# Kernel optimization log

Hardware: AMD Instinct MI355X
Metric: run time of the kernel (lower is better)

The kernel has to match this reference:

```python
import jax, jax.numpy as jnp
import numpy as np

G = 4      # groups (conv groups == offset groups)
KS = 3     # kernel size
DIL = 1    # dilation
PAD = 1    # padding = dilation
EPS = 1e-5 # InstanceNorm eps


def setup_inputs() -> dict:
    key = jax.random.key(0)
    k1, k2, k3, k4, k5 = jax.random.split(key, 5)
    B, C, D, H, W = 4, 64, 8, 64, 64
    Cout = 64
    Cg = C // G
    x = jax.random.normal(k1, (B, C, D, H, W), jnp.float32)
    # small offset-conv weights so predicted offsets stay within a few pixels
    w_off = jax.random.normal(k2, (2 * KS * KS * G, Cg, KS, KS), jnp.float32) * 0.01
    b_off = jax.random.normal(k3, (2 * KS * KS * G,), jnp.float32) * 0.01
    w_dc = jax.random.normal(k4, (Cout, Cg, KS, KS), jnp.float32) * (1.0 / np.sqrt(Cg * KS * KS))
    b_dc = jax.random.normal(k5, (Cout,), jnp.float32) * 0.01
    return {"x": x, "w_off": w_off, "b_off": b_off, "w_dc": w_dc, "b_dc": b_dc}


def reference(x, w_off, b_off, w_dc, b_dc):
    B, C, D, H, W = x.shape
    N = B * D
    K = KS * KS
    Cg = C // G
    # torch .view(B*D, C, H, W) is a row-major reshape of the flat buffer
    x2 = x.reshape(N, C, H, W)

    # grouped 3x3 offset conv, same padding
    off = jax.lax.conv_general_dilated(
        x2, w_off, (1, 1), [(PAD, PAD), (PAD, PAD)],
        rhs_dilation=(DIL, DIL), feature_group_count=G,
        dimension_numbers=("NCHW", "OIHW", "NCHW"),
    ) + b_off[None, :, None, None]
    off = off.reshape(N, G, K, 2, H, W)        # (y, x) offset per group/kernel-pt
    dy, dx = off[:, :, :, 0], off[:, :, :, 1]  # [N,G,K,H,W]

    # base sampling grid per kernel point
    ki, kj = jnp.meshgrid(jnp.arange(KS), jnp.arange(KS), indexing="ij")
    ki = ki.reshape(K); kj = kj.reshape(K)
    base_y = (jnp.arange(H)[None, :] - PAD + ki[:, None] * DIL).astype(jnp.float32)  # [K,H]
    base_x = (jnp.arange(W)[None, :] - PAD + kj[:, None] * DIL).astype(jnp.float32)  # [K,W]
    py = base_y[None, None, :, :, None] + dy   # [N,G,K,H,W]
    px = base_x[None, None, :, None, :] + dx

    y0 = jnp.floor(py); x0 = jnp.floor(px)
    ly = py - y0; lx = px - x0
    y0i = y0.astype(jnp.int32); x0i = x0.astype(jnp.int32)

    xg = x2.reshape(N, G, Cg, H * W)
    gather = jax.vmap(jax.vmap(lambda xf, idx: xf[:, idx]))  # over N, G

    def corner(yi, xi, w):
        valid = (yi >= 0) & (yi < H) & (xi >= 0) & (xi < W)   # zero-pad OOB
        idx = jnp.clip(yi, 0, H - 1) * W + jnp.clip(xi, 0, W - 1)
        v = gather(xg, idx.reshape(N, G, -1)).reshape(N, G, Cg, K, H, W)
        return v * (w * valid)[:, :, None]                    # broadcast over Cg

    val = (corner(y0i,     x0i,     (1 - ly) * (1 - lx))
         + corner(y0i,     x0i + 1, (1 - ly) * lx)
         + corner(y0i + 1, x0i,     ly * (1 - lx))
         + corner(y0i + 1, x0i + 1, ly * lx))                 # [N,G,Cg,K,H,W]

    wg = w_dc.reshape(G, -1, Cg, K)                           # [G,Coutg,Cg,K]
    out = jnp.einsum("gock,ngckhw->ngohw", wg, val).reshape(N, -1, H, W)
    out = out + b_dc[None, :, None, None]

    # InstanceNorm2d (affine=False, biased var) + exact GELU
    m = out.mean((-2, -1), keepdims=True)
    v = out.var((-2, -1), keepdims=True)
    out = jax.nn.gelu((out - m) * jax.lax.rsqrt(v + EPS), approximate=False)

    Cout = out.shape[1]
    return out.reshape(B, D, Cout, H, W).transpose(0, 2, 1, 3, 4)  # [B,Cout,D,H,W]
```

## Files before the change

kernel.cpp:

```cpp
#include <hip/hip_runtime.h>
#include <hip/hip_fp16.h>
#include <math.h>

#define HW 4096
#define NN 32
#define W68 68
#define RSTR 2192

typedef __attribute__((ext_vector_type(8))) _Float16 f16x8;
typedef __attribute__((ext_vector_type(2))) _Float16 h2;
typedef __attribute__((ext_vector_type(4))) float f32x4;

__device__ inline unsigned short hbits(float a) {
    _Float16 h = (_Float16)a;
    unsigned short u;
    __builtin_memcpy(&u, &h, 2);
    return u;
}
__device__ inline unsigned hpack(float a, float b) {
    auto p = __builtin_amdgcn_cvt_pkrtz(a, b);
    unsigned u;
    __builtin_memcpy(&u, &p, 4);
    return u;
}

__device__ inline int xsw(int x, int c8) {
    return ((x << 5) | (c8 << 4)) ^ (((x >> 2) & 1) << 4);
}

__global__ __launch_bounds__(256) void wperm_build(const float* __restrict__ w_off,
                                                   const float* __restrict__ w_dc,
                                                   unsigned short* __restrict__ wperm)
{
    int idx = blockIdx.x * 256 + threadIdx.x;
    int g = idx / 7680;
    int r3 = idx - g * 7680;
    int which = r3 / 2560;
    int r = r3 - which * 2560;
    int j = r & 7;
    int rest = r >> 3;
    int nn_ = rest & 15; rest >>= 4;
    int q_ = rest & 3, kp_ = rest >> 2;
    int k = q_ * 8 + j;
    int c = k & 15, tt = kp_ * 2 + (k >> 4);
    float v = 0.f;
    if (tt < 9) {
        if (which == 0)      v = w_dc[(g * 16 + nn_) * 144 + c * 9 + tt];
        else if (which == 1) v = w_off[(g * 18 + nn_) * 144 + c * 9 + tt];
        else if (nn_ < 2)    v = w_off[(g * 18 + 16 + nn_) * 144 + c * 9 + tt];
    }
    wperm[idx] = hbits(v);
}

__global__ __launch_bounds__(256, 4) void fused_conv(const float* __restrict__ x,
                                                     const unsigned short* __restrict__ wperm,
                                                     const float* __restrict__ b_off,
                                                     const float* __restrict__ b_dc,
                                                     unsigned short* __restrict__ outpre)
{
    __shared__ __attribute__((aligned(16))) unsigned short xwin[9864];
    __shared__ __attribute__((aligned(16))) unsigned short off_lds[256 * 20];

    int bhw = blockIdx.x;
    int bx = (bhw & 7) * 256 + (bhw >> 3);
    int n = bx >> 6, g = (bx >> 4) & 3, chunk = bx & 15;
    int t = threadIdx.x;
    int lane = t & 63, wv = t >> 6;
    int nn = lane & 15, q = lane >> 4;
    int t2 = q >> 1, chh = q & 1;
    int R0 = chunk * 4;

    const unsigned short* wpg = wperm + g * 7680;
    const float* xgbase = x + (size_t)(n * 64 + g * 16) * HW;

    {
        int col = lane;
        #pragma unroll
        for (int rr = 0; rr < 2; rr++) {
            int r = wv * 2 + rr;
            int h = R0 + r - 2;
            uint4 lo = {0, 0, 0, 0}, hi = {0, 0, 0, 0};
            if ((unsigned)h < 64u) {
                const float* xp = xgbase + h * 64 + col;
                float v[16];
                #pragma unroll
                for (int c = 0; c < 16; c++) v[c] = xp[(size_t)c * HW];
                lo.x = hpack(v[0], v[1]);  lo.y = hpack(v[2], v[3]);
                lo.z = hpack(v[4], v[5]);  lo.w = hpack(v[6], v[7]);
                hi.x = hpack(v[8], v[9]);  hi.y = hpack(v[10], v[11]);
                hi.z = hpack(v[12], v[13]); hi.w = hpack(v[14], v[15]);
            }
            *(uint4*)((char*)xwin + r * RSTR + xsw(col + 2, 0)) = lo;
            *(uint4*)((char*)xwin + r * RSTR + xsw(col + 2, 1)) = hi;
        }
        {
            int h = R0 + 6;
            unsigned a = 0, b = 0;
            if (h < 64) {
                const float* xp = xgbase + (size_t)(wv * 4) * HW + h * 64 + col;
                a = hpack(xp[0], xp[HW]);
                b = hpack(xp[2 * HW], xp[3 * HW]);
            }
            char* p = (char*)xwin + 8 * RSTR + xsw(col + 2, wv >> 1) + (wv & 1) * 8;
            *(unsigned*)p = a;
            *(unsigned*)(p + 4) = b;
        }
        if (t < 72) {
            int r = t >> 3, rem = t & 7;
            int xc = rem >> 1, c8 = rem & 1;
            int xx = xc < 2 ? xc : xc + 64;
            uint4 z = {0, 0, 0, 0};
            *(uint4*)((char*)xwin + r * RSTR + xsw(xx, c8)) = z;
        }
    }

    int pls[4]; float fy[4], fx[4]; int rws[4], xbs[4];
    #pragma unroll
    for (int s = 0; s < 4; s++) {
        int pl = (wv * 4 + s) * 16 + nn;
        int pos = chunk * 256 + pl;
        int h = pos >> 6, w = pos & 63;
        pls[s] = pl;
        fy[s] = (float)(h - 1);
        fx[s] = (float)(w - 1);
        rws[s] = ((wv * 4 + s) >> 2) + 1;
        xbs[s] = ((wv * 4 + s) & 3) * 16 + nn + 1;
    }

    __syncthreads();

    {
        f16x8 pb0[5], pb1[5];
        #pragma unroll
        for (int kp = 0; kp < 5; kp++) {
            int fo = ((kp * 4 + q) * 16 + nn) * 8;
            pb0[kp] = *(const f16x8*)(wpg + 2560 + fo);
            pb1[kp] = *(const f16x8*)(wpg + 5120 + fo);
        }

        f32x4 acc0[4], acc1[4];
        float bv0 = b_off[g * 18 + nn];
        float bv1 = (nn < 2) ? b_off[g * 18 + 16 + nn] : 0.f;
        #pragma unroll
        for (int s = 0; s < 4; s++)
            #pragma unroll
            for (int r = 0; r < 4; r++) { acc0[s][r] = bv0; acc1[s][r] = bv1; }

        uint4 xv[2][4];
        auto stage1 = [&](int kp) {
            int ki = t2 ? (2 * kp + 1) / 3 : (2 * kp) / 3;
            int kj = t2 ? (2 * kp + 1) % 3 : (2 * kp) % 3;
            int sl = kp & 1;
            #pragma unroll
            for (int s = 0; s < 4; s++) {
                int adr = (rws[s] + ki) * RSTR + xsw(xbs[s] + kj, chh);
                xv[sl][s] = *(const uint4*)((const char*)xwin + adr);
            }
        };
        stage1(0);
        #pragma unroll
        for (int kp = 0; kp < 5; kp++) {
            if (kp < 4) stage1(kp + 1);
            __builtin_amdgcn_sched_barrier(0);
            int sl = kp & 1;
            #pragma unroll
            for (int s = 0; s < 4; s++) {
                f16x8 af = *(f16x8*)&xv[sl][s];
                acc0[s] = __builtin_amdgcn_mfma_f32_16x16x32_f16(af, pb0[kp], acc0[s], 0, 0, 0);
                acc1[s] = __builtin_amdgcn_mfma_f32_16x16x32_f16(af, pb1[kp], acc1[s], 0, 0, 0);
            }
        }

        #pragma unroll
        for (int s = 0; s < 4; s++) {
            int pl = (wv * 4 + s) * 16 + q * 4;
            #pragma unroll
            for (int r = 0; r < 4; r++) {
                off_lds[(pl + r) * 20 + nn] = hbits(acc0[s][r]);
                if (nn < 2)
                    off_lds[(pl + r) * 20 + 16 + nn] = hbits(acc1[s][r]);
            }
        }
        off_lds[t * 20 + 18] = 0;
        off_lds[t * 20 + 19] = 0;
    }

    f16x8 bwr[5];
    #pragma unroll
    for (int kp = 0; kp < 5; kp++)
        bwr[kp] = *(const f16x8*)(wpg + ((kp * 4 + q) * 16 + nn) * 8);

    __syncthreads();

    f32x4 acc[4];
    float bv = b_dc[g * 16 + nn];
    #pragma unroll
    for (int s = 0; s < 4; s++)
        #pragma unroll
        for (int r = 0; r < 4; r++) acc[s][r] = bv;

    uint4 RA[2], RB[2], RC[2], RD[2];
    h2 rwh[2][4];
    int rinw[2], rgy[2], rgx[2];

    auto gather_x = [&](int R, int C) -> uint4 {
        uint4 out = {0, 0, 0, 0};
        int h = R - 2, w = C - 2;
        if ((unsigned)h < 64u && (unsigned)w < 64u) {
            const float* xp = xgbase + (size_t)(chh * 8) * HW + h * 64 + w;
            unsigned* o = (unsigned*)&out;
            #pragma unroll
            for (int k = 0; k < 4; k++)
                o[k] = hpack(xp[(size_t)(2 * k) * HW], xp[(size_t)(2 * k + 1) * HW]);
        }
        return out;
    };

    auto stage = [&](int u) {
        int kp = u >> 2, s = u & 3, sl = u & 1;
        int ki = t2 ? (2 * kp + 1) / 3 : (2 * kp) / 3;
        int kj = t2 ? (2 * kp + 1) % 3 : (2 * kp) % 3;
        unsigned uo = *(const unsigned*)&off_lds[pls[s] * 20 + 4 * kp + 2 * t2];
        h2 oo;
        __builtin_memcpy(&oo, &uo, 4);
        float py = fy[s] + (float)ki + (float)oo[0];
        float px = fx[s] + (float)kj + (float)oo[1];
        float y0f = fminf(fmaxf(floorf(py), -2.f), 64.f);
        float x0f = fminf(fmaxf(floorf(px), -2.f), 64.f);
        float ly = py - y0f, lx = px - x0f;
        float my = 1.f - ly, mx = 1.f - lx;
        rwh[sl][0] = h2{(_Float16)(my * mx), (_Float16)(my * mx)};
        rwh[sl][1] = h2{(_Float16)(my * lx), (_Float16)(my * lx)};
        rwh[sl][2] = h2{(_Float16)(ly * mx), (_Float16)(ly * mx)};
        rwh[sl][3] = h2{(_Float16)(ly * lx), (_Float16)(ly * lx)};
        int y0 = (int)y0f, x0 = (int)x0f;
        int lr = y0 + 2 - R0;
        int inw = ((unsigned)lr <= 7u);
        int lrc = inw ? lr : 0;
        int xx = x0 + 2;
        int a0 = lrc * RSTR + xsw(xx, chh);
        int a1 = lrc * RSTR + xsw(xx + 1, chh);
        RA[sl] = *(const uint4*)((const char*)xwin + a0);
        RB[sl] = *(const uint4*)((const char*)xwin + a1);
        RC[sl] = *(const uint4*)((const char*)xwin + a0 + RSTR);
        RD[sl] = *(const uint4*)((const char*)xwin + a1 + RSTR);
        rinw[sl] = inw;
        rgy[sl] = y0 + 2;
        rgx[sl] = xx;
    };
    auto consume = [&](int u) {
        int kp = u >> 2, s = u & 3, sl = u & 1;
        if (!__all(rinw[sl])) {
            if (!rinw[sl]) {
                int R = rgy[sl], C = rgx[sl];
                RA[sl] = gather_x(R, C);
                RB[sl] = gather_x(R, C + 1);
                RC[sl] = gather_x(R + 1, C);
                RD[sl] = gather_x(R + 1, C + 1);
            }
        }
        const h2* A2 = (const h2*)&RA[sl];
        const h2* B2 = (const h2*)&RB[sl];
        const h2* C2 = (const h2*)&RC[sl];
        const h2* D2 = (const h2*)&RD[sl];
        h2 w0 = rwh[sl][0], w1 = rwh[sl][1], w2 = rwh[sl][2], w3 = rwh[sl][3];
        uint4 afu;
        unsigned* au = (unsigned*)&afu;
        #pragma unroll
        for (int j = 0; j < 4; j++) {
            h2 v = w0 * A2[j] + w1 * B2[j] + w2 * C2[j] + w3 * D2[j];
            __builtin_memcpy(&au[j], &v, 4);
        }
        f16x8 af = *(f16x8*)&afu;
        acc[s] = __builtin_amdgcn_mfma_f32_16x16x32_f16(af, bwr[kp], acc[s], 0, 0, 0);
    };

    stage(0);
    #pragma unroll
    for (int u = 0; u < 20; u++) {
        if (u < 19) stage(u + 1);
        __builtin_amdgcn_sched_barrier(0);
        consume(u);
    }

    __syncthreads();
    #pragma unroll
    for (int s = 0; s < 4; s++) {
        int colb = (wv * 4 + s) * 16 + q * 4;
        uint2 pk;
        pk.x = hpack(acc[s][0], acc[s][1]);
        pk.y = hpack(acc[s][2], acc[s][3]);
        *(uint2*)(off_lds + nn * 264 + colb) = pk;
    }
    __syncthreads();
    unsigned short* opb = outpre + (size_t)(n * 64 + g * 16) * HW + chunk * 256;
    #pragma unroll
    for (int p = 0; p < 2; p++) {
        int idx = p * 256 + t;
        int ch = idx >> 5, slot = idx & 31;
        uint4 vv = *(const uint4*)(off_lds + ch * 264 + slot * 8);
        *(uint4*)(opb + (size_t)ch * HW + slot * 8) = vv;
    }
}

__global__ __launch_bounds__(256) void norm_gelu(const unsigned short* __restrict__ outpre,
                                                 float* __restrict__ out)
{
    __shared__ float red[8];
    int bhw = blockIdx.x;
    int bx = (bhw & 7) * 256 + (bhw >> 3);
    int n  = bx >> 6;
    int co = bx & 63;
    int t  = threadIdx.x;

    const uint2* base = (const uint2*)(outpre + (size_t)(n * 64 + co) * HW);
    float4 v[4];
    float s = 0.f, sq = 0.f;
    #pragma unroll
    for (int r = 0; r < 4; r++) {
        uint2 u2 = base[t + r * 256];
        h2 p0, p1;
        __builtin_memcpy(&p0, &u2.x, 4);
        __builtin_memcpy(&p1, &u2.y, 4);
        v[r].x = (float)p0[0]; v[r].y = (float)p0[1];
        v[r].z = (float)p1[0]; v[r].w = (float)p1[1];
        s  += v[r].x + v[r].y + v[r].z + v[r].w;
        sq  = fmaf(v[r].x, v[r].x, sq);
        sq  = fmaf(v[r].y, v[r].y, sq);
        sq  = fmaf(v[r].z, v[r].z, sq);
        sq  = fmaf(v[r].w, v[r].w, sq);
    }
    #pragma unroll
    for (int o2 = 32; o2 > 0; o2 >>= 1) {
        s  += __shfl_down(s,  o2, 64);
        sq += __shfl_down(sq, o2, 64);
    }
    int wid = t >> 6, lane = t & 63;
    if (lane == 0) { red[wid] = s; red[4 + wid] = sq; }
    __syncthreads();
    float S  = red[0] + red[1] + red[2] + red[3];
    float SQ = red[4] + red[5] + red[6] + red[7];
    float mean = S * (1.f / 4096.f);
    float var  = SQ * (1.f / 4096.f) - mean * mean;
    float rstd = rsqrtf(var + 1e-5f);

    int b = n >> 3, d = n & 7;
    float4* outp = (float4*)(out + ((size_t)(b * 64 + co) * 8 + d) * HW);
    #pragma unroll
    for (int r = 0; r < 4; r++) {
        float xs[4] = {v[r].x, v[r].y, v[r].z, v[r].w};
        float4 res;
        float* rp = (float*)&res;
        #pragma unroll
        for (int qq = 0; qq < 4; qq++) {
            float xn = (xs[qq] - mean) * rstd;
            float u = xn * (1.5957691f + 0.0713548162f * xn * xn);
            float e = __expf(-u);
            rp[qq] = xn * __frcp_rn(1.f + e);
        }
        outp[t + r * 256] = res;
    }
}

extern "C" void kernel_launch(void* const* d_in, const int* in_sizes, int n_in,
                              void* d_out, int out_size, void* d_ws, size_t ws_size,
                              hipStream_t stream) {
    const float* x     = (const float*)d_in[0];
    const float* w_off = (const float*)d_in[1];
    const float* w_dc  = (const float*)d_in[3];
    float* out = (float*)d_out;

    unsigned short* wperm = (unsigned short*)d_ws;
    unsigned short* outpre = (unsigned short*)((char*)d_ws + 61440);

    wperm_build<<<120, 256, 0, stream>>>(w_off, w_dc, wperm);
    fused_conv <<<2048, 256, 0, stream>>>(x, wperm,
                                          (const float*)d_in[2],
                                          (const float*)d_in[4], outpre);
    norm_gelu  <<<2048, 256, 0, stream>>>(outpre, out);
}
```

Measured before the change: 122.2 us.

## Process two row chunks per block to reuse a taller input halo window

```diff
diff --git a/kernel.cpp b/kernel.cpp
--- a/kernel.cpp
+++ b/kernel.cpp
@@ -58,17 +58,17 @@
                                                      const float* __restrict__ b_dc,
                                                      unsigned short* __restrict__ outpre)
 {
-    __shared__ __attribute__((aligned(16))) unsigned short xwin[9864];
+    __shared__ __attribute__((aligned(16))) unsigned short xwin[14248];
     __shared__ __attribute__((aligned(16))) unsigned short off_lds[256 * 20];
 
     int bhw = blockIdx.x;
-    int bx = (bhw & 7) * 256 + (bhw >> 3);
-    int n = bx >> 6, g = (bx >> 4) & 3, chunk = bx & 15;
+    int bx = (bhw & 7) * 128 + (bhw >> 3);
+    int n = bx >> 5, g = (bx >> 3) & 3, chunk2 = bx & 7;
     int t = threadIdx.x;
     int lane = t & 63, wv = t >> 6;
     int nn = lane & 15, q = lane >> 4;
     int t2 = q >> 1, chh = q & 1;
-    int R0 = chunk * 4;
+    int R0 = chunk2 * 8;
 
     const unsigned short* wpg = wperm + g * 7680;
     const float* xgbase = x + (size_t)(n * 64 + g * 16) * HW;
@@ -76,8 +76,8 @@
     {
         int col = lane;
         #pragma unroll
-        for (int rr = 0; rr < 2; rr++) {
-            int r = wv * 2 + rr;
+        for (int rr = 0; rr < 3; rr++) {
+            int r = wv * 3 + rr;
             int h = R0 + r - 2;
             uint4 lo = {0, 0, 0, 0}, hi = {0, 0, 0, 0};
             if ((unsigned)h < 64u) {
@@ -94,18 +94,18 @@
             *(uint4*)((char*)xwin + r * RSTR + xsw(col + 2, 1)) = hi;
         }
         {
-            int h = R0 + 6;
+            int h = R0 + 10;
             unsigned a = 0, b = 0;
             if (h < 64) {
                 const float* xp = xgbase + (size_t)(wv * 4) * HW + h * 64 + col;
                 a = hpack(xp[0], xp[HW]);
                 b = hpack(xp[2 * HW], xp[3 * HW]);
             }
-            char* p = (char*)xwin + 8 * RSTR + xsw(col + 2, wv >> 1) + (wv & 1) * 8;
+            char* p = (char*)xwin + 12 * RSTR + xsw(col + 2, wv >> 1) + (wv & 1) * 8;
             *(unsigned*)p = a;
             *(unsigned*)(p + 4) = b;
         }
-        if (t < 72) {
+        if (t < 104) {
             int r = t >> 3, rem = t & 7;
             int xc = rem >> 1, c8 = rem & 1;
             int xx = xc < 2 ? xc : xc + 64;
@@ -114,94 +114,29 @@
         }
     }
 
-    int pls[4]; float fy[4], fx[4]; int rws[4], xbs[4];
+    f16x8 pb0[5], pb1[5], bwr[5];
+    #pragma unroll
+    for (int kp = 0; kp < 5; kp++) {
+        int fo = ((kp * 4 + q) * 16 + nn) * 8;
+        pb0[kp] = *(const f16x8*)(wpg + 2560 + fo);
+        pb1[kp] = *(const f16x8*)(wpg + 5120 + fo);
+        bwr[kp] = *(const f16x8*)(wpg + fo);
+    }
+    float bv0 = b_off[g * 18 + nn];
+    float bv1 = (nn < 2) ? b_off[g * 18 + 16 + nn] : 0.f;
+    float bvd = b_dc[g * 16 + nn];
+
+    int pls[4], xbs[4]; float fx_[4];
     #pragma unroll
     for (int s = 0; s < 4; s++) {
         int pl = (wv * 4 + s) * 16 + nn;
-        int pos = chunk * 256 + pl;
-        int h = pos >> 6, w = pos & 63;
         pls[s] = pl;
-        fy[s] = (float)(h - 1);
-        fx[s] = (float)(w - 1);
-        rws[s] = ((wv * 4 + s) >> 2) + 1;
-        xbs[s] = ((wv * 4 + s) & 3) * 16 + nn + 1;
+        int w = ((wv * 4 + s) & 3) * 16 + nn;
+        fx_[s] = (float)(w - 1);
+        xbs[s] = w + 1;
     }
 
     __syncthreads();
-
-    {
-        f16x8 pb0[5], pb1[5];
-        #pragma unroll
-        for (int kp = 0; kp < 5; kp++) {
-            int fo = ((kp * 4 + q) * 16 + nn) * 8;
-            pb0[kp] = *(const f16x8*)(wpg + 2560 + fo);
-            pb1[kp] = *(const f16x8*)(wpg + 5120 + fo);
-        }
-
-        f32x4 acc0[4], acc1[4];
-        float bv0 = b_off[g * 18 + nn];
-        float bv1 = (nn < 2) ? b_off[g * 18 + 16 + nn] : 0.f;
-        #pragma unroll
-        for (int s = 0; s < 4; s++)
-            #pragma unroll
-            for (int r = 0; r < 4; r++) { acc0[s][r] = bv0; acc1[s][r] = bv1; }
-
-        uint4 xv[2][4];
-        auto stage1 = [&](int kp) {
-            int ki = t2 ? (2 * kp + 1) / 3 : (2 * kp) / 3;
-            int kj = t2 ? (2 * kp + 1) % 3 : (2 * kp) % 3;
-            int sl = kp & 1;
-            #pragma unroll
-            for (int s = 0; s < 4; s++) {
-                int adr = (rws[s] + ki) * RSTR + xsw(xbs[s] + kj, chh);
-                xv[sl][s] = *(const uint4*)((const char*)xwin + adr);
-            }
-        };
-        stage1(0);
-        #pragma unroll
-        for (int kp = 0; kp < 5; kp++) {
-            if (kp < 4) stage1(kp + 1);
-            __builtin_amdgcn_sched_barrier(0);
-            int sl = kp & 1;
-            #pragma unroll
-            for (int s = 0; s < 4; s++) {
-                f16x8 af = *(f16x8*)&xv[sl][s];
-                acc0[s] = __builtin_amdgcn_mfma_f32_16x16x32_f16(af, pb0[kp], acc0[s], 0, 0, 0);
-                acc1[s] = __builtin_amdgcn_mfma_f32_16x16x32_f16(af, pb1[kp], acc1[s], 0, 0, 0);
-            }
-        }
-
-        #pragma unroll
-        for (int s = 0; s < 4; s++) {
-            int pl = (wv * 4 + s) * 16 + q * 4;
-            #pragma unroll
-            for (int r = 0; r < 4; r++) {
-                off_lds[(pl + r) * 20 + nn] = hbits(acc0[s][r]);
-                if (nn < 2)
-                    off_lds[(pl + r) * 20 + 16 + nn] = hbits(acc1[s][r]);
-            }
-        }
-        off_lds[t * 20 + 18] = 0;
-        off_lds[t * 20 + 19] = 0;
-    }
-
-    f16x8 bwr[5];
-    #pragma unroll
-    for (int kp = 0; kp < 5; kp++)
-        bwr[kp] = *(const f16x8*)(wpg + ((kp * 4 + q) * 16 + nn) * 8);
-
-    __syncthreads();
-
-    f32x4 acc[4];
-    float bv = b_dc[g * 16 + nn];
-    #pragma unroll
-    for (int s = 0; s < 4; s++)
-        #pragma unroll
-        for (int r = 0; r < 4; r++) acc[s][r] = bv;
-
-    uint4 RA[2], RB[2], RC[2], RD[2];
-    h2 rwh[2][4];
-    int rinw[2], rgy[2], rgx[2];
 
     auto gather_x = [&](int R, int C) -> uint4 {
         uint4 out = {0, 0, 0, 0};
@@ -216,90 +151,155 @@
         return out;
     };
 
-    auto stage = [&](int u) {
-        int kp = u >> 2, s = u & 3, sl = u & 1;
-        int ki = t2 ? (2 * kp + 1) / 3 : (2 * kp) / 3;
-        int kj = t2 ? (2 * kp + 1) % 3 : (2 * kp) % 3;
-        unsigned uo = *(const unsigned*)&off_lds[pls[s] * 20 + 4 * kp + 2 * t2];
-        h2 oo;
-        __builtin_memcpy(&oo, &uo, 4);
-        float py = fy[s] + (float)ki + (float)oo[0];
-        float px = fx[s] + (float)kj + (float)oo[1];
-        float y0f = fminf(fmaxf(floorf(py), -2.f), 64.f);
-        float x0f = fminf(fmaxf(floorf(px), -2.f), 64.f);
-        float ly = py - y0f, lx = px - x0f;
-        float my = 1.f - ly, mx = 1.f - lx;
-        rwh[sl][0] = h2{(_Float16)(my * mx), (_Float16)(my * mx)};
-        rwh[sl][1] = h2{(_Float16)(my * lx), (_Float16)(my * lx)};
-        rwh[sl][2] = h2{(_Float16)(ly * mx), (_Float16)(ly * mx)};
-        rwh[sl][3] = h2{(_Float16)(ly * lx), (_Float16)(ly * lx)};
-        int y0 = (int)y0f, x0 = (int)x0f;
-        int lr = y0 + 2 - R0;
-        int inw = ((unsigned)lr <= 7u);
-        int lrc = inw ? lr : 0;
-        int xx = x0 + 2;
-        int a0 = lrc * RSTR + xsw(xx, chh);
-        int a1 = lrc * RSTR + xsw(xx + 1, chh);
-        RA[sl] = *(const uint4*)((const char*)xwin + a0);
-        RB[sl] = *(const uint4*)((const char*)xwin + a1);
-        RC[sl] = *(const uint4*)((const char*)xwin + a0 + RSTR);
-        RD[sl] = *(const uint4*)((const char*)xwin + a1 + RSTR);
-        rinw[sl] = inw;
-        rgy[sl] = y0 + 2;
-        rgx[sl] = xx;
-    };
-    auto consume = [&](int u) {
-        int kp = u >> 2, s = u & 3, sl = u & 1;
-        if (!__all(rinw[sl])) {
-            if (!rinw[sl]) {
-                int R = rgy[sl], C = rgx[sl];
-                RA[sl] = gather_x(R, C);
-                RB[sl] = gather_x(R, C + 1);
-                RC[sl] = gather_x(R + 1, C);
-                RD[sl] = gather_x(R + 1, C + 1);
-            }
-        }
-        const h2* A2 = (const h2*)&RA[sl];
-        const h2* B2 = (const h2*)&RB[sl];
-        const h2* C2 = (const h2*)&RC[sl];
-        const h2* D2 = (const h2*)&RD[sl];
-        h2 w0 = rwh[sl][0], w1 = rwh[sl][1], w2 = rwh[sl][2], w3 = rwh[sl][3];
-        uint4 afu;
-        unsigned* au = (unsigned*)&afu;
-        #pragma unroll
-        for (int j = 0; j < 4; j++) {
-            h2 v = w0 * A2[j] + w1 * B2[j] + w2 * C2[j] + w3 * D2[j];
-            __builtin_memcpy(&au[j], &v, 4);
-        }
-        f16x8 af = *(f16x8*)&afu;
-        acc[s] = __builtin_amdgcn_mfma_f32_16x16x32_f16(af, bwr[kp], acc[s], 0, 0, 0);
-    };
-
-    stage(0);
-    #pragma unroll
-    for (int u = 0; u < 20; u++) {
-        if (u < 19) stage(u + 1);
-        __builtin_amdgcn_sched_barrier(0);
-        consume(u);
-    }
-
-    __syncthreads();
-    #pragma unroll
-    for (int s = 0; s < 4; s++) {
-        int colb = (wv * 4 + s) * 16 + q * 4;
-        uint2 pk;
-        pk.x = hpack(acc[s][0], acc[s][1]);
-        pk.y = hpack(acc[s][2], acc[s][3]);
-        *(uint2*)(off_lds + nn * 264 + colb) = pk;
-    }
-    __syncthreads();
-    unsigned short* opb = outpre + (size_t)(n * 64 + g * 16) * HW + chunk * 256;
-    #pragma unroll
-    for (int p = 0; p < 2; p++) {
-        int idx = p * 256 + t;
-        int ch = idx >> 5, slot = idx & 31;
-        uint4 vv = *(const uint4*)(off_lds + ch * 264 + slot * 8);
-        *(uint4*)(opb + (size_t)ch * HW + slot * 8) = vv;
+    #pragma unroll
+    for (int ci = 0; ci < 2; ci++) {
+        if (ci) __syncthreads();
+        int rwbase = 4 * ci + wv + 1;
+        float fybase = (float)(R0 + 4 * ci + wv - 1);
+
+        {
+            f32x4 acc0[4], acc1[4];
+            #pragma unroll
+            for (int s = 0; s < 4; s++)
+                #pragma unroll
+                for (int r = 0; r < 4; r++) { acc0[s][r] = bv0; acc1[s][r] = bv1; }
+
+            uint4 xv[2][4];
+            auto stage1 = [&](int kp) {
+                int ki = t2 ? (2 * kp + 1) / 3 : (2 * kp) / 3;
+                int kj = t2 ? (2 * kp + 1) % 3 : (2 * kp) % 3;
+                int sl = kp & 1;
+                #pragma unroll
+                for (int s = 0; s < 4; s++) {
+                    int adr = (rwbase + ki) * RSTR + xsw(xbs[s] + kj, chh);
+                    xv[sl][s] = *(const uint4*)((const char*)xwin + adr);
+                }
+            };
+            stage1(0);
+            #pragma unroll
+            for (int kp = 0; kp < 5; kp++) {
+                if (kp < 4) stage1(kp + 1);
+                __builtin_amdgcn_sched_barrier(0);
+                int sl = kp & 1;
+                #pragma unroll
+                for (int s = 0; s < 4; s++) {
+                    f16x8 af = *(f16x8*)&xv[sl][s];
+                    acc0[s] = __builtin_amdgcn_mfma_f32_16x16x32_f16(af, pb0[kp], acc0[s], 0, 0, 0);
+                    acc1[s] = __builtin_amdgcn_mfma_f32_16x16x32_f16(af, pb1[kp], acc1[s], 0, 0, 0);
+                }
+            }
+
+            #pragma unroll
+            for (int s = 0; s < 4; s++) {
+                int pl = (wv * 4 + s) * 16 + q * 4;
+                #pragma unroll
+                for (int r = 0; r < 4; r++) {
+                    off_lds[(pl + r) * 20 + nn] = hbits(acc0[s][r]);
+                    if (nn < 2)
+                        off_lds[(pl + r) * 20 + 16 + nn] = hbits(acc1[s][r]);
+                }
+            }
+            off_lds[t * 20 + 18] = 0;
+            off_lds[t * 20 + 19] = 0;
+        }
+        __syncthreads();
+
+        f32x4 acc[4];
+        #pragma unroll
+        for (int s = 0; s < 4; s++)
+            #pragma unroll
+            for (int r = 0; r < 4; r++) acc[s][r] = bvd;
+
+        uint4 RA[2], RB[2], RC[2], RD[2];
+        h2 rwh[2][4];
+        int rinw[2], rgy[2], rgx[2];
+
+        auto stage = [&](int u) {
+            int kp = u >> 2, s = u & 3, sl = u & 1;
+            int ki = t2 ? (2 * kp + 1) / 3 : (2 * kp) / 3;
+            int kj = t2 ? (2 * kp + 1) % 3 : (2 * kp) % 3;
+            unsigned uo = *(const unsigned*)&off_lds[pls[s] * 20 + 4 * kp + 2 * t2];
+            h2 oo;
+            __builtin_memcpy(&oo, &uo, 4);
+            float py = fybase + (float)ki + (float)oo[0];
+            float px = fx_[s] + (float)kj + (float)oo[1];
+            float y0f = fminf(fmaxf(floorf(py), -2.f), 64.f);
+            float x0f = fminf(fmaxf(floorf(px), -2.f), 64.f);
+            float ly = py - y0f, lx = px - x0f;
+            float my = 1.f - ly, mx = 1.f - lx;
+            rwh[sl][0] = h2{(_Float16)(my * mx), (_Float16)(my * mx)};
+            rwh[sl][1] = h2{(_Float16)(my * lx), (_Float16)(my * lx)};
+            rwh[sl][2] = h2{(_Float16)(ly * mx), (_Float16)(ly * mx)};
+            rwh[sl][3] = h2{(_Float16)(ly * lx), (_Float16)(ly * lx)};
+            int y0 = (int)y0f, x0 = (int)x0f;
+            int lr = y0 + 2 - R0;
+            int inw = ((unsigned)lr <= 11u);
+            int lrc = inw ? lr : 0;
+            int xx = x0 + 2;
+            int a0 = lrc * RSTR + xsw(xx, chh);
+            int a1 = lrc * RSTR + xsw(xx + 1, chh);
+            RA[sl] = *(const uint4*)((const char*)xwin + a0);
+            RB[sl] = *(const uint4*)((const char*)xwin + a1);
+            RC[sl] = *(const uint4*)((const char*)xwin + a0 + RSTR);
+            RD[sl] = *(const uint4*)((const char*)xwin + a1 + RSTR);
+            rinw[sl] = inw;
+            rgy[sl] = y0 + 2;
+            rgx[sl] = xx;
+        };
+        auto consume = [&](int u) {
+            int kp = u >> 2, s = u & 3, sl = u & 1;
+            if (!__all(rinw[sl])) {
+                if (!rinw[sl]) {
+                    int R = rgy[sl], C = rgx[sl];
+                    RA[sl] = gather_x(R, C);
+                    RB[sl] = gather_x(R, C + 1);
+                    RC[sl] = gather_x(R + 1, C);
+                    RD[sl] = gather_x(R + 1, C + 1);
+                }
+            }
+            const h2* A2 = (const h2*)&RA[sl];
+            const h2* B2 = (const h2*)&RB[sl];
+            const h2* C2 = (const h2*)&RC[sl];
+            const h2* D2 = (const h2*)&RD[sl];
+            h2 w0 = rwh[sl][0], w1 = rwh[sl][1], w2 = rwh[sl][2], w3 = rwh[sl][3];
+            uint4 afu;
+            unsigned* au = (unsigned*)&afu;
+            #pragma unroll
+            for (int j = 0; j < 4; j++) {
+                h2 v = w0 * A2[j] + w1 * B2[j] + w2 * C2[j] + w3 * D2[j];
+                __builtin_memcpy(&au[j], &v, 4);
+            }
+            f16x8 af = *(f16x8*)&afu;
+            acc[s] = __builtin_amdgcn_mfma_f32_16x16x32_f16(af, bwr[kp], acc[s], 0, 0, 0);
+        };
+
+        stage(0);
+        #pragma unroll
+        for (int u = 0; u < 20; u++) {
+            if (u < 19) stage(u + 1);
+            __builtin_amdgcn_sched_barrier(0);
+            consume(u);
+        }
+
+        __syncthreads();
+        #pragma unroll
+        for (int s = 0; s < 4; s++) {
+            int colb = (wv * 4 + s) * 16 + q * 4;
+            uint2 pk;
+            pk.x = hpack(acc[s][0], acc[s][1]);
+            pk.y = hpack(acc[s][2], acc[s][3]);
+            *(uint2*)(off_lds + nn * 264 + colb) = pk;
+        }
+        __syncthreads();
+        unsigned short* opb = outpre + (size_t)(n * 64 + g * 16) * HW
+                            + (chunk2 * 2 + ci) * 256;
+        #pragma unroll
+        for (int p = 0; p < 2; p++) {
+            int idx = p * 256 + t;
+            int ch = idx >> 5, slot = idx & 31;
+            uint4 vv = *(const uint4*)(off_lds + ch * 264 + slot * 8);
+            *(uint4*)(opb + (size_t)ch * HW + slot * 8) = vv;
+        }
     }
 }
 
@@ -374,7 +374,7 @@
     unsigned short* outpre = (unsigned short*)((char*)d_ws + 61440);
 
     wperm_build<<<120, 256, 0, stream>>>(w_off, w_dc, wperm);
-    fused_conv <<<2048, 256, 0, stream>>>(x, wperm,
+    fused_conv <<<1024, 256, 0, stream>>>(x, wperm,
                                           (const float*)d_in[2],
                                           (const float*)d_in[4], outpre);
     norm_gelu  <<<2048, 256, 0, stream>>>(outpre, out);
```

Result: slower. 160.5 us (+31.3%).
